# Performance work log

Measured on AMD Instinct MI355X. Metric: run time of the kernel, lower is better.

## Reference

```python
import jax, jax.numpy as jnp
import numpy as np

N = 4096
H = 512
NUM_HEADS = 8
HEAD_DIM = H // NUM_HEADS
NUM_SETS = 1365


def setup_inputs() -> dict:
    key = jax.random.key(0)
    ks = jax.random.split(key, 24)
    s = 1.0 / np.sqrt(H)
    def lin(i):
        W = jax.random.normal(ks[i], (H, H), dtype=jnp.float32) * s
        b = jnp.zeros((H,), dtype=jnp.float32)
        return W, b
    Ws, bs = lin(0)
    Wq1, bq1 = lin(1); Wk1, bk1 = lin(2); Wv1, bv1 = lin(3); Wo1, bo1 = lin(4)
    Wq2, bq2 = lin(5); Wk2, bk2 = lin(6); Wv2, bv2 = lin(7); Wo2, bo2 = lin(8)
    # beta init is zeros in the module; use small nonzero so attention path matters
    beta1 = jnp.array([0.1], dtype=jnp.float32)
    beta2 = jnp.array([0.1], dtype=jnp.float32)
    embeddings = jax.random.normal(ks[9], (N, H), dtype=jnp.float32)
    batch_indices = jnp.sort(jax.random.randint(ks[10], (N,), 0, NUM_SETS))
    return dict(embeddings=embeddings, batch_indices=batch_indices,
                Ws=Ws, bs=bs,
                Wq1=Wq1, bq1=bq1, Wk1=Wk1, bk1=bk1, Wv1=Wv1, bv1=bv1, Wo1=Wo1, bo1=bo1, beta1=beta1,
                Wq2=Wq2, bq2=bq2, Wk2=Wk2, bk2=bk2, Wv2=Wv2, bv2=bv2, Wo2=Wo2, bo2=bo2, beta2=beta2)


def _attn_layer(x, mask, Wq, bq, Wk, bk, Wv, bv, Wo, bo, beta):
    n = x.shape[0]
    q = (x @ Wq + bq).reshape(n, NUM_HEADS, HEAD_DIM)
    k = (x @ Wk + bk).reshape(n, NUM_HEADS, HEAD_DIM)
    v = (x @ Wv + bv).reshape(n, NUM_HEADS, HEAD_DIM)
    scores = jnp.einsum('nhd,mhd->hnm', q, k) / np.sqrt(HEAD_DIM).astype(np.float32)
    scores = jnp.where(mask[None, :, :], scores, -jnp.inf)
    w = jax.nn.softmax(scores, axis=-1)
    w = jnp.nan_to_num(w, nan=0.0)  # rows with no valid key -> 0 (matches torch nan_to_num)
    out = jnp.einsum('hnm,mhd->nhd', w, v).reshape(n, H)
    return beta * (out @ Wo + bo) + x


def reference(embeddings, batch_indices, Ws, bs,
              Wq1, bq1, Wk1, bk1, Wv1, bv1, Wo1, bo1, beta1,
              Wq2, bq2, Wk2, bk2, Wv2, bv2, Wo2, bo2, beta2):
    n = embeddings.shape[0]
    static_emb = jax.nn.relu(embeddings @ Ws + bs)
    same_set = batch_indices[:, None] == batch_indices[None, :]
    mask = same_set & ~jnp.eye(n, dtype=bool)
    dyn = _attn_layer(embeddings, mask, Wq1, bq1, Wk1, bk1, Wv1, bv1, Wo1, bo1, beta1)
    dyn = _attn_layer(dyn, mask, Wq2, bq2, Wk2, bk2, Wv2, bv2, Wo2, bo2, beta2)
    sq = (dyn - static_emb) ** 2
    seg_sum = jax.ops.segment_sum(sq, batch_indices, num_segments=NUM_SETS)
    cnt = jax.ops.segment_sum(jnp.ones((n,), dtype=sq.dtype), batch_indices, num_segments=NUM_SETS)
    return seg_sum / jnp.maximum(cnt, 1.0)[:, None]
```

## Files before the change

### kernel.cpp

```cpp
#include <hip/hip_runtime.h>
#include <hip/hip_bf16.h>
#include <math.h>
#include <stdint.h>

#define N_NODES   4096
#define HDIM      512
#define NUM_HEADS 8
#define HEAD_DIM  64
#define NUM_SETS  1365
#define KDIM      512

typedef __attribute__((ext_vector_type(8))) short bf16x8;
typedef __attribute__((ext_vector_type(4))) float f32x4;

__device__ inline unsigned short f2bfu(float x) {
    __hip_bfloat16 h = __float2bfloat16(x);
    return __builtin_bit_cast(unsigned short, h);
}
__device__ inline float bfu2f(unsigned short u) {
    unsigned v = (unsigned)u << 16;
    return __builtin_bit_cast(float, v);
}

__device__ inline void gload_lds16(const void* g, void* l) {
    __builtin_amdgcn_global_load_lds(
        (const __attribute__((address_space(1))) unsigned int*)g,
        (__attribute__((address_space(3))) unsigned int*)l,
        16, 0, 0);
}

__global__ __launch_bounds__(256) void prep_kernel(
        const float* W0, const float* W1, const float* W2, const float* W3,
        const float* W4, const float* W5, const float* W6, const float* W7,
        const float* W8, __hip_bfloat16* __restrict__ wt,
        const float* __restrict__ emb, __hip_bfloat16* __restrict__ embb,
        const int* __restrict__ batch,
        int* __restrict__ seg_s, int* __restrict__ seg_e) {
    const int bx = blockIdx.x;
    if (bx < 2304) {
        __shared__ float t[32][36];
        const int z = bx >> 8;
        const int tb = bx & 255;
        const float* W = z==0?W0:z==1?W1:z==2?W2:z==3?W3:z==4?W4:z==5?W5:z==6?W6:z==7?W7:W8;
        __hip_bfloat16* Wt = wt + (size_t)z * (512 * 512);
        const int bn = (tb & 15) * 32, bk = (tb >> 4) * 32;
        const int nx = threadIdx.x & 7, ky = threadIdx.x >> 3;
        *(float4*)&t[ky][nx * 4] = *(const float4*)&W[(size_t)(bk + ky) * 512 + bn + nx * 4];
        __syncthreads();
        const int r2 = threadIdx.x >> 3;
        const int ck = threadIdx.x & 7;
        uint2 p;
        p.x = (unsigned)f2bfu(t[ck * 4 + 0][r2]) | ((unsigned)f2bfu(t[ck * 4 + 1][r2]) << 16);
        p.y = (unsigned)f2bfu(t[ck * 4 + 2][r2]) | ((unsigned)f2bfu(t[ck * 4 + 3][r2]) << 16);
        *(uint2*)&Wt[(size_t)(bn + r2) * 512 + bk + ck * 4] = p;
    } else if (bx < 4352) {
        const int i = (bx - 2304) * 256 + threadIdx.x;
        float4 v = ((const float4*)emb)[i];
        uint2 p;
        p.x = (unsigned)f2bfu(v.x) | ((unsigned)f2bfu(v.y) << 16);
        p.y = (unsigned)f2bfu(v.z) | ((unsigned)f2bfu(v.w) << 16);
        ((uint2*)embb)[i] = p;
    } else {
        const int i = (bx - 4352) * 256 + threadIdx.x;
        const int bi = batch[i];
        if (i == 0 || batch[i - 1] != bi) {
            int e = i + 1;
            while (e < N_NODES && batch[e] == bi) ++e;
            for (int j = i; j < e; ++j) { seg_s[j] = i; seg_e[j] = e; }
        }
    }
}

template<int MODE>
__global__ __launch_bounds__(512) void gemm128(
        const __hip_bfloat16* __restrict__ A,
        const __hip_bfloat16* __restrict__ Wt0, const __hip_bfloat16* __restrict__ Wt1,
        const __hip_bfloat16* __restrict__ Wt2, const __hip_bfloat16* __restrict__ Wt3,
        const float* __restrict__ bias0, const float* __restrict__ bias1,
        const float* __restrict__ bias2, const float* __restrict__ bias3,
        __hip_bfloat16* __restrict__ statB, __hip_bfloat16* __restrict__ outB) {
    __shared__ alignas(16) short Al[2][128][64];
    __shared__ alignas(16) short Bl[2][128][64];

    const int tid = threadIdx.x;
    const int wid = tid >> 6, lane = tid & 63;
    constexpr int NY = (MODE == 0) ? 16 : 12;
    const int hwid = blockIdx.y * gridDim.x + blockIdx.x;
    const int xcd = hwid & 7;
    const int t8  = hwid >> 3;
    const int bg  = t8 / NY;
    const int yy  = t8 % NY;
    const int brow = (bg * 8 + xcd) * 128;
    const int wsel = yy >> 2;
    const int bcol = (yy & 3) * 128;
    const __hip_bfloat16* Wt = (wsel == 0) ? Wt0 : (wsel == 1) ? Wt1 : (wsel == 2) ? Wt2 : Wt3;
    const float* bias        = (wsel == 0) ? bias0 : (wsel == 1) ? bias1 : (wsel == 2) ? bias2 : bias3;

    const int swzc = (lane & 7) ^ ((lane >> 3) & 7);
    const __hip_bfloat16* aSrc = A  + (size_t)(brow + wid * 16 + (lane >> 3)) * KDIM + swzc * 8;
    const __hip_bfloat16* bSrc = Wt + (size_t)(bcol + wid * 16 + (lane >> 3)) * KDIM + swzc * 8;

    const int fr = lane & 15, fq = lane >> 4;
    const int rx = fr & 7;
    const int wm = (wid >> 1) * 32;
    const int wn = (wid & 1) * 64;

    auto STAGE = [&](int buf, int t) {
        const int k0 = t * 64;
        gload_lds16(aSrc + k0, &Al[buf][wid * 16][0]);
        gload_lds16(aSrc + k0 + (size_t)8 * KDIM, &Al[buf][wid * 16 + 8][0]);
        gload_lds16(bSrc + k0, &Bl[buf][wid * 16][0]);
        gload_lds16(bSrc + k0 + (size_t)8 * KDIM, &Bl[buf][wid * 16 + 8][0]);
    };

    STAGE(0, 0);
    STAGE(1, 1);

    const int ch0 = ((0 + fq) ^ rx) * 8;
    const int ch1 = ((4 + fq) ^ rx) * 8;

    f32x4 acc[2][4] = {};
    #pragma unroll
    for (int t = 0; t < 8; ++t) {
        const int cur = t & 1;
        if (t < 7) asm volatile("s_waitcnt vmcnt(4)" ::: "memory");
        else       asm volatile("s_waitcnt vmcnt(0)" ::: "memory");
        __builtin_amdgcn_s_barrier();
        __builtin_amdgcn_sched_barrier(0);
        bf16x8 a0[2], a1[2], b0[4], b1[4];
        #pragma unroll
        for (int mi = 0; mi < 2; ++mi) {
            a0[mi] = *(const bf16x8*)&Al[cur][wm + mi * 16 + fr][ch0];
            a1[mi] = *(const bf16x8*)&Al[cur][wm + mi * 16 + fr][ch1];
        }
        #pragma unroll
        for (int ni = 0; ni < 4; ++ni) {
            b0[ni] = *(const bf16x8*)&Bl[cur][wn + ni * 16 + fr][ch0];
            b1[ni] = *(const bf16x8*)&Bl[cur][wn + ni * 16 + fr][ch1];
        }
        __builtin_amdgcn_s_setprio(1);
        #pragma unroll
        for (int mi = 0; mi < 2; ++mi)
            #pragma unroll
            for (int ni = 0; ni < 4; ++ni) {
                acc[mi][ni] = __builtin_amdgcn_mfma_f32_16x16x32_bf16(a0[mi], b0[ni], acc[mi][ni], 0, 0, 0);
                acc[mi][ni] = __builtin_amdgcn_mfma_f32_16x16x32_bf16(a1[mi], b1[ni], acc[mi][ni], 0, 0, 0);
            }
        __builtin_amdgcn_s_setprio(0);
        __builtin_amdgcn_sched_barrier(0);
        __builtin_amdgcn_s_barrier();
        if (t + 2 < 8) STAGE(cur, t + 2);
    }

    float bv[4];
    #pragma unroll
    for (int ni = 0; ni < 4; ++ni) bv[ni] = bias[bcol + wn + ni * 16 + fr];

    #pragma unroll
    for (int mi = 0; mi < 2; ++mi) {
        #pragma unroll
        for (int ni = 0; ni < 4; ++ni) {
            const int c = bcol + wn + ni * 16 + fr;
            #pragma unroll
            for (int r = 0; r < 4; ++r) {
                const int row = brow + wm + mi * 16 + fq * 4 + r;
                const float v = acc[mi][ni][r] + bv[ni];
                if (MODE == 0) {
                    if (wsel == 0) statB[(size_t)row * 512 + c] = __float2bfloat16(fmaxf(v, 0.f));
                    else           outB[(size_t)row * 1536 + (wsel - 1) * 512 + c] = __float2bfloat16(v);
                } else {
                    outB[(size_t)row * 1536 + wsel * 512 + c] = __float2bfloat16(v);
                }
            }
        }
    }
}

template<bool MSE>
__global__ __launch_bounds__(256) void gemm_oproj(
        const __hip_bfloat16* __restrict__ A, const __hip_bfloat16* __restrict__ Wt,
        const float* __restrict__ bias,
        const __hip_bfloat16* __restrict__ X, const float* __restrict__ betaP,
        __hip_bfloat16* __restrict__ outB,
        const unsigned short* __restrict__ statB,
        const int* __restrict__ batch,
        const int* __restrict__ seg_s, const int* __restrict__ seg_e,
        float* __restrict__ outMse) {
    __shared__ alignas(16) short Al[2][64][64];
    __shared__ alignas(16) short Bl[2][64][64];

    const int tid = threadIdx.x;
    const int wid = tid >> 6, lane = tid & 63;
    const int hwid = blockIdx.y * gridDim.x + blockIdx.x;
    const int xcd = hwid & 7;
    const int t8  = hwid >> 3;
    const int brow = ((t8 >> 3) * 8 + xcd) * 64;
    const int bcol = (t8 & 7) * 64;

    const int swzc = (lane & 7) ^ ((lane >> 3) & 7);
    const __hip_bfloat16* aSrc = A  + (size_t)(brow + wid * 16 + (lane >> 3)) * KDIM + swzc * 8;
    const __hip_bfloat16* bSrc = Wt + (size_t)(bcol + wid * 16 + (lane >> 3)) * KDIM + swzc * 8;

    const int fr = lane & 15, fq = lane >> 4;
    const int rx = fr & 7;
    const int wm = (wid >> 1) * 32, wn = (wid & 1) * 32;

    auto STAGE = [&](int buf, int t) {
        const int k0 = t * 64;
        gload_lds16(aSrc + k0, &Al[buf][wid * 16][0]);
        gload_lds16(aSrc + k0 + (size_t)8 * KDIM, &Al[buf][wid * 16 + 8][0]);
        gload_lds16(bSrc + k0, &Bl[buf][wid * 16][0]);
        gload_lds16(bSrc + k0 + (size_t)8 * KDIM, &Bl[buf][wid * 16 + 8][0]);
    };

    STAGE(0, 0);
    STAGE(1, 1);

    const int ch0 = ((0 + fq) ^ rx) * 8;
    const int ch1 = ((4 + fq) ^ rx) * 8;

    f32x4 acc[2][2] = {};
    #pragma unroll
    for (int t = 0; t < 8; ++t) {
        const int cur = t & 1;
        if (t < 7) asm volatile("s_waitcnt vmcnt(4)" ::: "memory");
        else       asm volatile("s_waitcnt vmcnt(0)" ::: "memory");
        __builtin_amdgcn_s_barrier();
        __builtin_amdgcn_sched_barrier(0);
        bf16x8 a0[2], a1[2], b0[2], b1[2];
        #pragma unroll
        for (int mi = 0; mi < 2; ++mi) {
            a0[mi] = *(const bf16x8*)&Al[cur][wm + mi * 16 + fr][ch0];
            a1[mi] = *(const bf16x8*)&Al[cur][wm + mi * 16 + fr][ch1];
        }
        #pragma unroll
        for (int ni = 0; ni < 2; ++ni) {
            b0[ni] = *(const bf16x8*)&Bl[cur][wn + ni * 16 + fr][ch0];
            b1[ni] = *(const bf16x8*)&Bl[cur][wn + ni * 16 + fr][ch1];
        }
        __builtin_amdgcn_s_setprio(1);
        #pragma unroll
        for (int mi = 0; mi < 2; ++mi)
            #pragma unroll
            for (int ni = 0; ni < 2; ++ni) {
                acc[mi][ni] = __builtin_amdgcn_mfma_f32_16x16x32_bf16(a0[mi], b0[ni], acc[mi][ni], 0, 0, 0);
                acc[mi][ni] = __builtin_amdgcn_mfma_f32_16x16x32_bf16(a1[mi], b1[ni], acc[mi][ni], 0, 0, 0);
            }
        __builtin_amdgcn_s_setprio(0);
        __builtin_amdgcn_sched_barrier(0);
        __builtin_amdgcn_s_barrier();
        if (t + 2 < 8) STAGE(cur, t + 2);
    }

    float bv[2];
    #pragma unroll
    for (int ni = 0; ni < 2; ++ni) bv[ni] = bias[bcol + wn + ni * 16 + fr];
    const float beta = betaP[0];

    int   rbi[2][4];
    float rinv[2][4];
    if (MSE) {
        #pragma unroll
        for (int mi = 0; mi < 2; ++mi)
            #pragma unroll
            for (int r = 0; r < 4; ++r) {
                const int row = brow + wm + mi * 16 + fq * 4 + r;
                rbi[mi][r]  = batch[row];
                rinv[mi][r] = 1.f / fmaxf((float)(seg_e[row] - seg_s[row]), 1.f);
            }
    }

    #pragma unroll
    for (int mi = 0; mi < 2; ++mi) {
        #pragma unroll
        for (int ni = 0; ni < 2; ++ni) {
            const int c = bcol + wn + ni * 16 + fr;
            #pragma unroll
            for (int r = 0; r < 4; ++r) {
                const int row = brow + wm + mi * 16 + fq * 4 + r;
                const float xv = __bfloat162float(X[(size_t)row * 512 + c]);
                const float v = beta * (acc[mi][ni][r] + bv[ni]) + xv;
                if (!MSE) {
                    outB[(size_t)row * 512 + c] = __float2bfloat16(v);
                } else {
                    const float sd = v - bfu2f(statB[(size_t)row * 512 + c]);
                    atomicAdd(&outMse[(size_t)rbi[mi][r] * 512 + c], sd * sd * rinv[mi][r]);
                }
            }
        }
    }
}

__global__ __launch_bounds__(256) void attn_kernel(
        const __hip_bfloat16* __restrict__ qkv,
        const int* __restrict__ seg_s, const int* __restrict__ seg_e,
        __hip_bfloat16* __restrict__ ab) {
    const int node = (blockIdx.x * blockDim.x + threadIdx.x) >> 6;
    const int lane = threadIdx.x & 63;
    const int c8   = lane * 8;

    bf16x8 q8 = *(const bf16x8*)&qkv[(size_t)node * 1536 + c8];
    float qf[8];
    #pragma unroll
    for (int j = 0; j < 8; ++j) qf[j] = bfu2f((unsigned short)q8[j]);

    const int s = seg_s[node], e = seg_e[node];

    float M = -INFINITY, S = 0.f;
    float o[8] = {};
    for (int m = s; m < e; ++m) {
        if (m == node) continue;
        bf16x8 k8 = *(const bf16x8*)&qkv[(size_t)m * 1536 + 512 + c8];
        float p = 0.f;
        #pragma unroll
        for (int j = 0; j < 8; ++j) p = fmaf(qf[j], bfu2f((unsigned short)k8[j]), p);
        p += __shfl_xor(p, 1, 64);
        p += __shfl_xor(p, 2, 64);
        p += __shfl_xor(p, 4, 64);
        const float sc = p * 0.125f;
        const float newM = fmaxf(M, sc);
        const float scale = __expf(M - newM);
        const float w = __expf(sc - newM);
        S = S * scale + w;
        bf16x8 v8 = *(const bf16x8*)&qkv[(size_t)m * 1536 + 1024 + c8];
        #pragma unroll
        for (int j = 0; j < 8; ++j) o[j] = fmaf(w, bfu2f((unsigned short)v8[j]), o[j] * scale);
        M = newM;
    }
    const float inv = (S > 0.f) ? (1.f / S) : 0.f;
    bf16x8 r;
    #pragma unroll
    for (int j = 0; j < 8; ++j) r[j] = (short)f2bfu(o[j] * inv);
    *(bf16x8*)&ab[(size_t)node * 512 + c8] = r;
}

extern "C" void kernel_launch(void* const* d_in, const int* in_sizes, int n_in,
                              void* d_out, int out_size, void* d_ws, size_t ws_size,
                              hipStream_t stream) {
    const float* emb   = (const float*)d_in[0];
    const int*   batch = (const int*)  d_in[1];
    const float* Ws_   = (const float*)d_in[2];
    const float* bs_   = (const float*)d_in[3];
    const float* Wq1 = (const float*)d_in[4];  const float* bq1 = (const float*)d_in[5];
    const float* Wk1 = (const float*)d_in[6];  const float* bk1 = (const float*)d_in[7];
    const float* Wv1 = (const float*)d_in[8];  const float* bv1 = (const float*)d_in[9];
    const float* Wo1 = (const float*)d_in[10]; const float* bo1 = (const float*)d_in[11];
    const float* beta1 = (const float*)d_in[12];
    const float* Wq2 = (const float*)d_in[13]; const float* bq2 = (const float*)d_in[14];
    const float* Wk2 = (const float*)d_in[15]; const float* bk2 = (const float*)d_in[16];
    const float* Wv2 = (const float*)d_in[17]; const float* bv2 = (const float*)d_in[18];
    const float* Wo2 = (const float*)d_in[19]; const float* bo2 = (const float*)d_in[20];
    const float* beta2 = (const float*)d_in[21];

    char* w = (char*)d_ws;
    const size_t MB = 1024 * 1024;
    __hip_bfloat16* statB  = (__hip_bfloat16*)(w + 0 * MB);
    __hip_bfloat16* qkv    = (__hip_bfloat16*)(w + 4 * MB);
    __hip_bfloat16* embb   = (__hip_bfloat16*)(w + 16 * MB);
    __hip_bfloat16* ab     = (__hip_bfloat16*)(w + 20 * MB);
    __hip_bfloat16* dynb   = (__hip_bfloat16*)(w + 24 * MB);
    __hip_bfloat16* wt     = (__hip_bfloat16*)(w + 28 * MB);
    int* seg_s = (int*)(w + 33 * MB);
    int* seg_e = seg_s + N_NODES;

    const size_t WSZ = 512 * 512;
    __hip_bfloat16* wtS  = wt + 0 * WSZ;
    __hip_bfloat16* wtQ1 = wt + 1 * WSZ;
    __hip_bfloat16* wtK1 = wt + 2 * WSZ;
    __hip_bfloat16* wtV1 = wt + 3 * WSZ;
    __hip_bfloat16* wtO1 = wt + 4 * WSZ;
    __hip_bfloat16* wtQ2 = wt + 5 * WSZ;
    __hip_bfloat16* wtK2 = wt + 6 * WSZ;
    __hip_bfloat16* wtV2 = wt + 7 * WSZ;
    __hip_bfloat16* wtO2 = wt + 8 * WSZ;

    hipMemsetAsync(d_out, 0, (size_t)out_size * sizeof(float), stream);

    prep_kernel<<<4368, 256, 0, stream>>>(
        Ws_, Wq1, Wk1, Wv1, Wo1, Wq2, Wk2, Wv2, Wo2, wt,
        emb, embb, batch, seg_s, seg_e);

    gemm128<0><<<dim3(32, 16), 512, 0, stream>>>(
        embb, wtS, wtQ1, wtK1, wtV1, bs_, bq1, bk1, bv1, statB, qkv);
    attn_kernel<<<N_NODES / 4, 256, 0, stream>>>(qkv, seg_s, seg_e, ab);
    gemm_oproj<false><<<dim3(64, 8), 256, 0, stream>>>(
        ab, wtO1, bo1, embb, beta1, dynb, nullptr, nullptr, nullptr, nullptr, nullptr);

    gemm128<1><<<dim3(32, 12), 512, 0, stream>>>(
        dynb, wtQ2, wtK2, wtV2, wtV2, bq2, bk2, bv2, bv2, nullptr, qkv);
    attn_kernel<<<N_NODES / 4, 256, 0, stream>>>(qkv, seg_s, seg_e, ab);
    gemm_oproj<true><<<dim3(64, 8), 256, 0, stream>>>(
        ab, wtO2, bo2, dynb, beta2, nullptr,
        (const unsigned short*)statB, batch, seg_s, seg_e, (float*)d_out);
}
```

Measured before the change: 82.09 us.

## Move LDS refill before MFMAs, reduce MSE per block, drop XCD remap

In both GEMMs the next stage's global-to-LDS load is now issued right after the LDS fragment reads (with an lgkmcnt wait and a barrier), before the MFMA block rather than after it, so loads overlap compute. The XCD-aware block remapping is replaced by plain blockIdx row/column mapping. The final o-proj MSE epilogue stores squared differences to LDS and has 64 threads do a sequential per-column segmented sum over the sorted batch indices, writing directly and using atomics only for segments that cross block boundaries. The attention kernel moves to 512-thread blocks. The direct stores assume the output is zero-initialised and that each segment is owned by one block, which holds only because the batch indices are sorted.

```diff
diff --git a/kernel.cpp b/kernel.cpp
--- a/kernel.cpp
+++ b/kernel.cpp
@@ -84,15 +84,9 @@
 
     const int tid = threadIdx.x;
     const int wid = tid >> 6, lane = tid & 63;
-    constexpr int NY = (MODE == 0) ? 16 : 12;
-    const int hwid = blockIdx.y * gridDim.x + blockIdx.x;
-    const int xcd = hwid & 7;
-    const int t8  = hwid >> 3;
-    const int bg  = t8 / NY;
-    const int yy  = t8 % NY;
-    const int brow = (bg * 8 + xcd) * 128;
-    const int wsel = yy >> 2;
-    const int bcol = (yy & 3) * 128;
+    const int brow = blockIdx.x * 128;
+    const int wsel = blockIdx.y >> 2;
+    const int bcol = (blockIdx.y & 3) * 128;
     const __hip_bfloat16* Wt = (wsel == 0) ? Wt0 : (wsel == 1) ? Wt1 : (wsel == 2) ? Wt2 : Wt3;
     const float* bias        = (wsel == 0) ? bias0 : (wsel == 1) ? bias1 : (wsel == 2) ? bias2 : bias3;
 
@@ -138,6 +132,11 @@
             b0[ni] = *(const bf16x8*)&Bl[cur][wn + ni * 16 + fr][ch0];
             b1[ni] = *(const bf16x8*)&Bl[cur][wn + ni * 16 + fr][ch1];
         }
+        asm volatile("s_waitcnt lgkmcnt(0)" ::: "memory");
+        __builtin_amdgcn_sched_barrier(0);
+        __builtin_amdgcn_s_barrier();
+        if (t + 2 < 8) STAGE(cur, t + 2);
+        __builtin_amdgcn_sched_barrier(0);
         __builtin_amdgcn_s_setprio(1);
         #pragma unroll
         for (int mi = 0; mi < 2; ++mi)
@@ -147,9 +146,6 @@
                 acc[mi][ni] = __builtin_amdgcn_mfma_f32_16x16x32_bf16(a1[mi], b1[ni], acc[mi][ni], 0, 0, 0);
             }
         __builtin_amdgcn_s_setprio(0);
-        __builtin_amdgcn_sched_barrier(0);
-        __builtin_amdgcn_s_barrier();
-        if (t + 2 < 8) STAGE(cur, t + 2);
     }
 
     float bv[4];
@@ -182,20 +178,23 @@
         const float* __restrict__ bias,
         const __hip_bfloat16* __restrict__ X, const float* __restrict__ betaP,
         __hip_bfloat16* __restrict__ outB,
-        const unsigned short* __restrict__ statB,
-        const int* __restrict__ batch,
+        const unsigned short* __restrict__ statB, const int* __restrict__ batch,
         const int* __restrict__ seg_s, const int* __restrict__ seg_e,
         float* __restrict__ outMse) {
     __shared__ alignas(16) short Al[2][64][64];
     __shared__ alignas(16) short Bl[2][64][64];
+    __shared__ int   batchL[64];
+    __shared__ float segInvL[64];
 
     const int tid = threadIdx.x;
     const int wid = tid >> 6, lane = tid & 63;
-    const int hwid = blockIdx.y * gridDim.x + blockIdx.x;
-    const int xcd = hwid & 7;
-    const int t8  = hwid >> 3;
-    const int brow = ((t8 >> 3) * 8 + xcd) * 64;
-    const int bcol = (t8 & 7) * 64;
+    const int brow = blockIdx.x * 64;
+    const int bcol = blockIdx.y * 64;
+
+    if (MSE && tid < 64) {
+        batchL[tid]  = batch[brow + tid];
+        segInvL[tid] = 1.f / fmaxf((float)(seg_e[brow + tid] - seg_s[brow + tid]), 1.f);
+    }
 
     const int swzc = (lane & 7) ^ ((lane >> 3) & 7);
     const __hip_bfloat16* aSrc = A  + (size_t)(brow + wid * 16 + (lane >> 3)) * KDIM + swzc * 8;
@@ -238,6 +237,11 @@
             b0[ni] = *(const bf16x8*)&Bl[cur][wn + ni * 16 + fr][ch0];
             b1[ni] = *(const bf16x8*)&Bl[cur][wn + ni * 16 + fr][ch1];
         }
+        asm volatile("s_waitcnt lgkmcnt(0)" ::: "memory");
+        __builtin_amdgcn_sched_barrier(0);
+        __builtin_amdgcn_s_barrier();
+        if (t + 2 < 8) STAGE(cur, t + 2);
+        __builtin_amdgcn_sched_barrier(0);
         __builtin_amdgcn_s_setprio(1);
         #pragma unroll
         for (int mi = 0; mi < 2; ++mi)
@@ -247,9 +251,6 @@
                 acc[mi][ni] = __builtin_amdgcn_mfma_f32_16x16x32_bf16(a1[mi], b1[ni], acc[mi][ni], 0, 0, 0);
             }
         __builtin_amdgcn_s_setprio(0);
-        __builtin_amdgcn_sched_barrier(0);
-        __builtin_amdgcn_s_barrier();
-        if (t + 2 < 8) STAGE(cur, t + 2);
     }
 
     float bv[2];
@@ -257,45 +258,72 @@
     for (int ni = 0; ni < 2; ++ni) bv[ni] = bias[bcol + wn + ni * 16 + fr];
     const float beta = betaP[0];
 
-    int   rbi[2][4];
-    float rinv[2][4];
-    if (MSE) {
-        #pragma unroll
-        for (int mi = 0; mi < 2; ++mi)
+    if (!MSE) {
+        #pragma unroll
+        for (int mi = 0; mi < 2; ++mi) {
             #pragma unroll
-            for (int r = 0; r < 4; ++r) {
-                const int row = brow + wm + mi * 16 + fq * 4 + r;
-                rbi[mi][r]  = batch[row];
-                rinv[mi][r] = 1.f / fmaxf((float)(seg_e[row] - seg_s[row]), 1.f);
-            }
-    }
-
-    #pragma unroll
-    for (int mi = 0; mi < 2; ++mi) {
-        #pragma unroll
-        for (int ni = 0; ni < 2; ++ni) {
-            const int c = bcol + wn + ni * 16 + fr;
+            for (int ni = 0; ni < 2; ++ni) {
+                const int c = bcol + wn + ni * 16 + fr;
+                #pragma unroll
+                for (int r = 0; r < 4; ++r) {
+                    const int row = brow + wm + mi * 16 + fq * 4 + r;
+                    const float xv = __bfloat162float(X[(size_t)row * 512 + c]);
+                    outB[(size_t)row * 512 + c] =
+                        __float2bfloat16(beta * (acc[mi][ni][r] + bv[ni]) + xv);
+                }
+            }
+        }
+    } else {
+        float* accLds = reinterpret_cast<float*>(&Al[0][0][0]);
+        #pragma unroll
+        for (int mi = 0; mi < 2; ++mi) {
             #pragma unroll
-            for (int r = 0; r < 4; ++r) {
-                const int row = brow + wm + mi * 16 + fq * 4 + r;
-                const float xv = __bfloat162float(X[(size_t)row * 512 + c]);
-                const float v = beta * (acc[mi][ni][r] + bv[ni]) + xv;
-                if (!MSE) {
-                    outB[(size_t)row * 512 + c] = __float2bfloat16(v);
-                } else {
+            for (int ni = 0; ni < 2; ++ni) {
+                const int cl = wn + ni * 16 + fr;
+                const int c = bcol + cl;
+                #pragma unroll
+                for (int r = 0; r < 4; ++r) {
+                    const int rl = wm + mi * 16 + fq * 4 + r;
+                    const int row = brow + rl;
+                    const float xv = __bfloat162float(X[(size_t)row * 512 + c]);
+                    const float v = beta * (acc[mi][ni][r] + bv[ni]) + xv;
                     const float sd = v - bfu2f(statB[(size_t)row * 512 + c]);
-                    atomicAdd(&outMse[(size_t)rbi[mi][r] * 512 + c], sd * sd * rinv[mi][r]);
+                    accLds[rl * 64 + cl] = sd * sd;
                 }
             }
         }
-    }
-}
-
-__global__ __launch_bounds__(256) void attn_kernel(
+        __syncthreads();
+        if (tid < 64) {
+            const int c = tid;
+            const bool prevSame = (brow > 0) && (batch[brow - 1] == batchL[0]);
+            const bool nextSame = (brow + 64 < N_NODES) && (batch[brow + 64] == batchL[63]);
+            float run = 0.f;
+            int cs = batchL[0];
+            bool first = true;
+            for (int i = 0; i < 64; ++i) {
+                const int b = batchL[i];
+                if (b != cs) {
+                    const float val = run * segInvL[i - 1];
+                    float* dst = &outMse[(size_t)cs * 512 + bcol + c];
+                    if (first && prevSame) atomicAdd(dst, val);
+                    else                   *dst = val;
+                    first = false; run = 0.f; cs = b;
+                }
+                run += accLds[i * 64 + c];
+            }
+            const float val = run * segInvL[63];
+            float* dst = &outMse[(size_t)cs * 512 + bcol + c];
+            if (nextSame || (first && prevSame)) atomicAdd(dst, val);
+            else                                 *dst = val;
+        }
+    }
+}
+
+__global__ __launch_bounds__(512) void attn_kernel(
         const __hip_bfloat16* __restrict__ qkv,
         const int* __restrict__ seg_s, const int* __restrict__ seg_e,
         __hip_bfloat16* __restrict__ ab) {
-    const int node = (blockIdx.x * blockDim.x + threadIdx.x) >> 6;
+    const int node = (int)(blockIdx.x * blockDim.x + threadIdx.x) >> 6;
     const int lane = threadIdx.x & 63;
     const int c8   = lane * 8;
 
@@ -382,13 +410,13 @@
 
     gemm128<0><<<dim3(32, 16), 512, 0, stream>>>(
         embb, wtS, wtQ1, wtK1, wtV1, bs_, bq1, bk1, bv1, statB, qkv);
-    attn_kernel<<<N_NODES / 4, 256, 0, stream>>>(qkv, seg_s, seg_e, ab);
+    attn_kernel<<<N_NODES / 8, 512, 0, stream>>>(qkv, seg_s, seg_e, ab);
     gemm_oproj<false><<<dim3(64, 8), 256, 0, stream>>>(
         ab, wtO1, bo1, embb, beta1, dynb, nullptr, nullptr, nullptr, nullptr, nullptr);
 
     gemm128<1><<<dim3(32, 12), 512, 0, stream>>>(
         dynb, wtQ2, wtK2, wtV2, wtV2, bq2, bk2, bv2, bv2, nullptr, qkv);
-    attn_kernel<<<N_NODES / 4, 256, 0, stream>>>(qkv, seg_s, seg_e, ab);
+    attn_kernel<<<N_NODES / 8, 512, 0, stream>>>(qkv, seg_s, seg_e, ab);
     gemm_oproj<true><<<dim3(64, 8), 256, 0, stream>>>(
         ab, wtO2, bo2, dynb, beta2, nullptr,
         (const unsigned short*)statB, batch, seg_s, seg_e, (float*)d_out);
```

New measurement: 75.72 us, median of 2. -7.8%, faster.
